# Kernel tuning notes

Hardware: AMD Instinct MI355X
Metric: run time of the kernel (lower is better)

Reference implementation:

```python
import jax, jax.numpy as jnp
import numpy as np

B, T, C, H = 32, 256, 512, 512
T_OUT = 8 * T  # fixed padded expanded length (max duration per token = 8)
ALPHA = 1.0
EPS = 1e-5


def _layer_norm(x, g, b):
    mu = jnp.mean(x, axis=-1, keepdims=True)
    var = jnp.mean(jnp.square(x - mu), axis=-1, keepdims=True)
    return (x - mu) * jax.lax.rsqrt(var + EPS) * g + b


def _conv1d_same(x, w, b):
    # x: [B,T,Cin], w: [3,Cin,Cout] -> [B,T,Cout]
    y = jax.lax.conv_general_dilated(x, w, window_strides=(1,), padding='SAME',
                                     dimension_numbers=('NWC', 'WIO', 'NWC'))
    return y + b


def setup_inputs() -> dict:
    key = jax.random.key(0)
    ks = jax.random.split(key, 8)
    s1 = 1.0 / np.sqrt(3 * C)
    s2 = 1.0 / np.sqrt(3 * H)
    return {
        'x': jax.random.normal(ks[0], (B, T, C), jnp.float32),
        'true_durations': jax.random.randint(ks[1], (B, T), 0, 8, jnp.int32),
        'W1': jax.random.normal(ks[2], (3, C, H), jnp.float32) * s1,
        'b1': jnp.zeros((H,), jnp.float32),
        'g1': jnp.ones((H,), jnp.float32),
        'beta1': jnp.zeros((H,), jnp.float32),
        'W2': jax.random.normal(ks[3], (3, H, H), jnp.float32) * s2,
        'b2': jnp.zeros((H,), jnp.float32),
        'g2': jnp.ones((H,), jnp.float32),
        'beta2': jnp.zeros((H,), jnp.float32),
        'Wl': jax.random.normal(ks[4], (H, 1), jnp.float32) * (1.0 / np.sqrt(H)),
        'bl': jnp.zeros((1,), jnp.float32),
    }


def _duration_predictor(x, W1, b1, g1, beta1, W2, b2, g2, beta2, Wl, bl):
    h = jax.nn.relu(_layer_norm(_conv1d_same(x, W1, b1), g1, beta1))
    h = jax.nn.relu(_layer_norm(_conv1d_same(h, W2, b2), g2, beta2))
    return (h @ Wl + bl)[..., 0]  # [B,T]


def _expand_by_durations(x, dur):
    # cumsum-based gather: output position t takes source token i where
    # csum[i-1] <= t < csum[i]; positions >= total length are zero-padded.
    csum = jnp.cumsum(dur, axis=-1)  # [B,T]
    pos = jnp.arange(T_OUT, dtype=csum.dtype)  # [T_OUT]
    idx = jax.vmap(lambda c: jnp.searchsorted(c, pos, side='right'))(csum)  # [B,T_OUT]
    valid = pos[None, :] < csum[:, -1:]
    idx = jnp.clip(idx, 0, dur.shape[1] - 1)
    out = jnp.take_along_axis(x, idx[..., None], axis=1)  # [B,T_OUT,C]
    return out * valid[..., None].astype(x.dtype)


def reference(x, true_durations, W1, b1, g1, beta1, W2, b2, g2, beta2, Wl, bl):
    log_lengths = _duration_predictor(x, W1, b1, g1, beta1, W2, b2, g2, beta2, Wl, bl) * ALPHA
    res = _expand_by_durations(x, true_durations)
    return res, log_lengths
```

## Files before the change

### kernel.cpp

```cpp
#include <hip/hip_runtime.h>
#include <hip/hip_bf16.h>

#define B_    32
#define T_    256
#define C_    512
#define H_    512
#define TOUT_ 2048
#define TP_   258
#define K_    1536
#define EPS_  1e-5f

typedef __attribute__((ext_vector_type(8))) short bf16x8;
typedef __attribute__((ext_vector_type(4))) float f32x4;

#define GLL16(g, l)                                                        \
  __builtin_amdgcn_global_load_lds(                                        \
      (const __attribute__((address_space(1))) void*)(g),                  \
      (__attribute__((address_space(3))) void*)(l), 16, 0, 0)

__device__ __forceinline__ void wt_convert_block(const float* __restrict__ W,
                                                 __hip_bfloat16* __restrict__ Wt,
                                                 int k0, int n0, int tid,
                                                 float* tile ) {
  const int tx = tid & 31;
  const int ty = tid >> 5;
#pragma unroll
  for (int i = 0; i < 4; ++i)
    tile[(ty * 4 + i) * 33 + tx] = W[(size_t)(k0 + ty * 4 + i) * H_ + n0 + tx];
  __syncthreads();
#pragma unroll
  for (int i = 0; i < 4; ++i)
    Wt[(size_t)(n0 + ty * 4 + i) * K_ + k0 + tx] =
        __float2bfloat16(tile[tx * 33 + ty * 4 + i]);
}

__device__ __forceinline__ void csum_block(const int* __restrict__ dur,
                                           int* __restrict__ csum,
                                           int b, int tid, int* wsum) {
  int v = dur[b * T_ + tid];
#pragma unroll
  for (int off = 1; off < 64; off <<= 1) {
    int u = __shfl_up(v, off);
    if ((tid & 63) >= off) v += u;
  }
  if ((tid & 63) == 63) wsum[tid >> 6] = v;
  __syncthreads();
  int base = 0;
#pragma unroll
  for (int j = 0; j < 4; ++j)
    if (j < (tid >> 6)) base += wsum[j];
  csum[b * T_ + tid] = v + base;
}

__device__ __forceinline__ void expand_copy_block(const float* __restrict__ X,
                                                  const int* __restrict__ csum,
                                                  float* __restrict__ res,
                                                  int u, int tid) {
  const int wave = (tid >> 6) & 3, lane = tid & 63;
#pragma unroll
  for (int k = 0; k < 4; ++k) {
    const int sr = u * 16 + wave * 4 + k;
    const int b = sr >> 8, t = sr & 255;
    const int* cb = csum + b * T_;
    const int c0 = t ? cb[t - 1] : 0;
    const int d  = cb[t] - c0;
    if (d == 0) continue;
    const float* src = X + (size_t)sr * C_;
    const float4 v0 = *(const float4*)(src + lane * 4);
    const float4 v1 = *(const float4*)(src + 256 + lane * 4);
    float* dst = res + ((size_t)b * TOUT_ + c0) * C_;
    for (int j = 0; j < d; ++j) {
      *(float4*)(dst + (size_t)j * C_ + lane * 4)       = v0;
      *(float4*)(dst + (size_t)j * C_ + 256 + lane * 4) = v1;
    }
  }
}

__device__ __forceinline__ void expand_zero_block(const int* __restrict__ csum,
                                                  float* __restrict__ res,
                                                  int z, int tid) {
  const int b  = z >> 6;
  const int t0 = (z & 63) << 5;
  const int total = csum[b * T_ + 255];
  const float4 z4 = make_float4(0.f, 0.f, 0.f, 0.f);
  const int half = (tid >> 7) & 1, c4 = tid & 127;
#pragma unroll
  for (int rr = half; rr < 32; rr += 2) {
    const int r = t0 + rr;
    if (r >= total)
      *(float4*)(res + ((size_t)b * TOUT_ + r) * C_ + c4 * 4) = z4;
  }
}

__global__ __launch_bounds__(256) void prep_kernel(const float* __restrict__ X,
                                                   const float* __restrict__ W1,
                                                   const int* __restrict__ dur,
                                                   __hip_bfloat16* __restrict__ xpad,
                                                   __hip_bfloat16* __restrict__ hpad,
                                                   __hip_bfloat16* __restrict__ Wt1,
                                                   int* __restrict__ csum) {
  __shared__ float tile[32 * 33];
  const int tid = threadIdx.x;
  if (blockIdx.x >= 4896) {
    csum_block(dur, csum, blockIdx.x - 4896, tid, (int*)tile);
    return;
  }
  if (blockIdx.x >= 4128) {
    const int id = blockIdx.x - 4128;
    wt_convert_block(W1, Wt1, (id % 48) * 32, (id / 48) * 32, tid, tile);
    return;
  }
  const int row = blockIdx.x * 2 + (tid >> 7);
  const int b = row / TP_;
  const int t = row - b * TP_;
  const int c = (tid & 127) * 4;
  __hip_bfloat16* dst = xpad + (size_t)row * C_ + c;
  if (t == 0 || t == TP_ - 1) {
    ushort4 zz = make_ushort4(0, 0, 0, 0);
    *(ushort4*)dst = zz;
    *(ushort4*)(hpad + (size_t)row * C_ + c) = zz;
    return;
  }
  const float4 v = *(const float4*)(X + (size_t)(b * T_ + t - 1) * C_ + c);
  union { __hip_bfloat16 h[4]; ushort4 u; } o;
  o.h[0] = __float2bfloat16(v.x);
  o.h[1] = __float2bfloat16(v.y);
  o.h[2] = __float2bfloat16(v.z);
  o.h[3] = __float2bfloat16(v.w);
  *(ushort4*)dst = o.u;
}

__global__ __launch_bounds__(512) void conv_expand_kernel(
    const __hip_bfloat16* __restrict__ Apad,
    const __hip_bfloat16* __restrict__ Wt,
    const float* __restrict__ bias,
    __hip_bfloat16* __restrict__ Y,
    const float* __restrict__ X,
    const int* __restrict__ csum,
    float* __restrict__ res,
    const float* __restrict__ W2,
    __hip_bfloat16* __restrict__ Wt2,
    int ex_base) {
  __shared__ __hip_bfloat16 smA[2][2][4096];
  __shared__ __hip_bfloat16 smB[2][2][4096];

  const int tid = threadIdx.x;

  if (blockIdx.x >= 896) {
    const int id = (blockIdx.x - 896) * 2 + (tid >> 8);
    float* tile = (float*)smA + (tid >> 8) * (32 * 33);
    wt_convert_block(W2, Wt2, (id % 48) * 32, (id / 48) * 32, tid & 255, tile);
    return;
  }
  if (blockIdx.x >= 256) {
    const int u = ex_base + (blockIdx.x - 256) * 2 + (tid >> 8);
    const int st = tid & 255;
    if (u < 512) expand_copy_block(X, csum, res, u, st);
    else         expand_zero_block(csum, res, u - 512, st);
    return;
  }

  const int lane = tid & 63;
  const int wid  = tid >> 6;
  const int cid  = blockIdx.x;
  const int n0 = (cid & 3) << 7;
  const int m0 = (cid >> 2) << 7;
  const int b  = m0 >> 8;
  const int t0 = m0 & 255;
  const int wm = (wid >> 2) << 6;
  const int wn = (wid & 3) << 5;

  const int rowS = tid >> 2;
  const int gsw  = ((tid & 3) + rowS) & 3;
  const __hip_bfloat16* arowA = Apad + (size_t)(b * TP_ + t0 + rowS) * C_ + (gsw << 3);
  const __hip_bfloat16* browB = Wt + (size_t)(n0 + rowS) * K_ + (gsw << 3);

  f32x4 acc[4][2] = {};

  auto stage = [&](int buf, int k0) {
    const int kw = k0 >> 9;
    const int c0 = k0 & 511;
    const __hip_bfloat16* a0 = arowA + kw * C_ + c0;
    GLL16(a0,           &smA[buf][0][tid << 3]);
    GLL16(a0 + 32,      &smA[buf][1][tid << 3]);
    GLL16(browB + k0,      &smB[buf][0][tid << 3]);
    GLL16(browB + k0 + 32, &smB[buf][1][tid << 3]);
  };

  auto compute = [&](int buf) {
    const int g   = lane >> 4;
    const int r15 = lane & 15;
    const int sa  = ((g - r15) & 3) << 3;
#pragma unroll
    for (int sl = 0; sl < 2; ++sl) {
      const __hip_bfloat16* As = smA[buf][sl];
      const __hip_bfloat16* Bs = smB[buf][sl];
      bf16x8 aF[4], bF[2];
#pragma unroll
      for (int i = 0; i < 4; ++i)
        aF[i] = *(const bf16x8*)(As + ((wm + (i << 4) + r15) << 5) + sa);
#pragma unroll
      for (int i = 0; i < 2; ++i)
        bF[i] = *(const bf16x8*)(Bs + ((wn + (i << 4) + r15) << 5) + sa);
#pragma unroll
      for (int mi = 0; mi < 4; ++mi)
#pragma unroll
        for (int ni = 0; ni < 2; ++ni)
          acc[mi][ni] = __builtin_amdgcn_mfma_f32_16x16x32_bf16(
              aF[mi], bF[ni], acc[mi][ni], 0, 0, 0);
    }
  };

  asm volatile("s_waitcnt vmcnt(0)" ::: "memory");
  stage(0, 0);
  stage(1, 64);

  for (int s = 0; s < 22; ++s) {
    asm volatile("s_waitcnt vmcnt(4)" ::: "memory");
    __builtin_amdgcn_sched_barrier(0);
    __builtin_amdgcn_s_barrier();
    compute(s & 1);
    asm volatile("s_waitcnt lgkmcnt(0)" ::: "memory");
    __builtin_amdgcn_s_barrier();
    stage(s & 1, (s + 2) << 6);
  }
  asm volatile("s_waitcnt vmcnt(4)" ::: "memory");
  __builtin_amdgcn_sched_barrier(0);
  __builtin_amdgcn_s_barrier();
  compute(0);
  asm volatile("s_waitcnt vmcnt(0)" ::: "memory");
  __builtin_amdgcn_sched_barrier(0);
  __builtin_amdgcn_s_barrier();
  compute(1);

  const int cn_base = n0 + wn + (lane & 15);
  const int rm_base = m0 + wm + ((lane >> 4) << 2);
#pragma unroll
  for (int ni = 0; ni < 2; ++ni) {
    const int cn = cn_base + (ni << 4);
    const float bb = bias[cn];
#pragma unroll
    for (int mi = 0; mi < 4; ++mi) {
#pragma unroll
      for (int rq = 0; rq < 4; ++rq) {
        const int rm = rm_base + (mi << 4) + rq;
        Y[(size_t)rm * H_ + cn] = __float2bfloat16(acc[mi][ni][rq] + bb);
      }
    }
  }
}

__global__ __launch_bounds__(256) void ln_relu_pad_kernel(
    const __hip_bfloat16* __restrict__ in,
    const float* __restrict__ g,
    const float* __restrict__ beta,
    __hip_bfloat16* __restrict__ outpad) {
  const int wave = threadIdx.x >> 6;
  const int lane = threadIdx.x & 63;
  const int row  = blockIdx.x * 4 + wave;

  const bf16x8 hv = *(const bf16x8*)(in + (size_t)row * H_ + lane * 8);
  const __hip_bfloat16* hh = (const __hip_bfloat16*)&hv;
  float f[8];
#pragma unroll
  for (int j = 0; j < 8; ++j) f[j] = __bfloat162float(hh[j]);

  float s = 0.f, q = 0.f;
#pragma unroll
  for (int j = 0; j < 8; ++j) { s += f[j]; q += f[j] * f[j]; }
#pragma unroll
  for (int off = 32; off; off >>= 1) {
    s += __shfl_xor(s, off);
    q += __shfl_xor(q, off);
  }
  const float mu  = s * (1.0f / 512.0f);
  const float var = q * (1.0f / 512.0f) - mu * mu;
  const float rs  = rsqrtf(var + EPS_);

  const float4 g0 = *(const float4*)(g + lane * 8);
  const float4 g1 = *(const float4*)(g + lane * 8 + 4);
  const float4 e0 = *(const float4*)(beta + lane * 8);
  const float4 e1 = *(const float4*)(beta + lane * 8 + 4);
  const float gg[8] = {g0.x, g0.y, g0.z, g0.w, g1.x, g1.y, g1.z, g1.w};
  const float ee[8] = {e0.x, e0.y, e0.z, e0.w, e1.x, e1.y, e1.z, e1.w};

  union { __hip_bfloat16 h[8]; bf16x8 v; } o;
#pragma unroll
  for (int j = 0; j < 8; ++j)
    o.h[j] = __float2bfloat16(fmaxf(0.f, (f[j] - mu) * rs * gg[j] + ee[j]));

  const int bq = row >> 8, t = row & 255;
  *(bf16x8*)(outpad + (size_t)(bq * TP_ + t + 1) * H_ + lane * 8) = o.v;
}

__global__ __launch_bounds__(256) void ln_relu_linear_kernel(
    const __hip_bfloat16* __restrict__ in,
    const float* __restrict__ g,
    const float* __restrict__ beta,
    const float* __restrict__ Wl,
    const float* __restrict__ bl,
    float* __restrict__ out) {
  const int wave = threadIdx.x >> 6;
  const int lane = threadIdx.x & 63;
  const int row  = blockIdx.x * 4 + wave;

  const bf16x8 hv = *(const bf16x8*)(in + (size_t)row * H_ + lane * 8);
  const __hip_bfloat16* hh = (const __hip_bfloat16*)&hv;
  float f[8];
#pragma unroll
  for (int j = 0; j < 8; ++j) f[j] = __bfloat162float(hh[j]);

  float s = 0.f, q = 0.f;
#pragma unroll
  for (int j = 0; j < 8; ++j) { s += f[j]; q += f[j] * f[j]; }
#pragma unroll
  for (int off = 32; off; off >>= 1) {
    s += __shfl_xor(s, off);
    q += __shfl_xor(q, off);
  }
  const float mu  = s * (1.0f / 512.0f);
  const float var = q * (1.0f / 512.0f) - mu * mu;
  const float rs  = rsqrtf(var + EPS_);

  const float4 g0 = *(const float4*)(g + lane * 8);
  const float4 g1 = *(const float4*)(g + lane * 8 + 4);
  const float4 e0 = *(const float4*)(beta + lane * 8);
  const float4 e1 = *(const float4*)(beta + lane * 8 + 4);
  const float4 w0 = *(const float4*)(Wl + lane * 8);
  const float4 w1 = *(const float4*)(Wl + lane * 8 + 4);
  const float gg[8] = {g0.x, g0.y, g0.z, g0.w, g1.x, g1.y, g1.z, g1.w};
  const float ee[8] = {e0.x, e0.y, e0.z, e0.w, e1.x, e1.y, e1.z, e1.w};
  const float ww[8] = {w0.x, w0.y, w0.z, w0.w, w1.x, w1.y, w1.z, w1.w};

  float sd = 0.f;
#pragma unroll
  for (int j = 0; j < 8; ++j)
    sd += fmaxf(0.f, (f[j] - mu) * rs * gg[j] + ee[j]) * ww[j];
#pragma unroll
  for (int off = 32; off; off >>= 1) sd += __shfl_xor(sd, off);

  if (lane == 0) out[row] = sd + bl[0];
}

extern "C" void kernel_launch(void* const* d_in, const int* in_sizes, int n_in,
                              void* d_out, int out_size, void* d_ws, size_t ws_size,
                              hipStream_t stream) {
  const float* x     = (const float*)d_in[0];
  const int*   dur   = (const int*)d_in[1];
  const float* W1    = (const float*)d_in[2];
  const float* b1    = (const float*)d_in[3];
  const float* g1    = (const float*)d_in[4];
  const float* beta1 = (const float*)d_in[5];
  const float* W2    = (const float*)d_in[6];
  const float* b2    = (const float*)d_in[7];
  const float* g2    = (const float*)d_in[8];
  const float* beta2 = (const float*)d_in[9];
  const float* Wl    = (const float*)d_in[10];
  const float* bl    = (const float*)d_in[11];

  float* out = (float*)d_out;
  float* res    = out;
  float* loglen = out + (size_t)B_ * TOUT_ * C_;

  char* ws = (char*)d_ws;
  __hip_bfloat16* xpad = (__hip_bfloat16*)ws;
  __hip_bfloat16* hpad = xpad + (size_t)B_ * TP_ * C_;
  __hip_bfloat16* Wt1  = hpad + (size_t)B_ * TP_ * C_;
  __hip_bfloat16* Wt2  = Wt1 + (size_t)H_ * K_;
  __hip_bfloat16* tmp  = Wt2 + (size_t)H_ * K_;
  int*   csum = (int*)(tmp + (size_t)B_ * T_ * H_);

  prep_kernel<<<4928, 256, 0, stream>>>(x, W1, dur, xpad, hpad, Wt1, csum);

  conv_expand_kernel<<<1280, 512, 0, stream>>>(xpad, Wt1, b1, tmp,
                                               x, csum, res, W2, Wt2, 0);
  ln_relu_pad_kernel<<<B_ * T_ / 4, 256, 0, stream>>>(tmp, g1, beta1, hpad);

  conv_expand_kernel<<<896, 512, 0, stream>>>(hpad, Wt2, b2, tmp,
                                              x, csum, res, nullptr, nullptr, 1280);
  ln_relu_linear_kernel<<<B_ * T_ / 4, 256, 0, stream>>>(tmp, g2, beta2, Wl, bl, loglen);
}
```

Before: 79.95 us.

## Use 256-thread blocks with 64x64 warp tiles in conv GEMM

The fused conv/expand kernel moves from 512-thread blocks with 8 waves of 64x32 tiles to 256-thread blocks with 4 waves of 64x64 tiles. Each wave now holds a 4x4 accumulator grid, which raises MFMA work per LDS fragment load. Each thread issues twice as many global-to-LDS loads, with the vmcnt waits and LDS swizzle adjusted to match. The expand and weight-convert side blocks now handle one unit per block, so the grid sizes grow. In exchange, register pressure rises and fewer waves per CU are available to hide latency.

```diff
diff --git a/kernel.cpp b/kernel.cpp
--- a/kernel.cpp
+++ b/kernel.cpp
@@ -130,7 +130,7 @@
   *(ushort4*)dst = o.u;
 }
 
-__global__ __launch_bounds__(512) void conv_expand_kernel(
+__global__ __launch_bounds__(256) void conv_expand_kernel(
     const __hip_bfloat16* __restrict__ Apad,
     const __hip_bfloat16* __restrict__ Wt,
     const float* __restrict__ bias,
@@ -146,17 +146,15 @@
 
   const int tid = threadIdx.x;
 
-  if (blockIdx.x >= 896) {
-    const int id = (blockIdx.x - 896) * 2 + (tid >> 8);
-    float* tile = (float*)smA + (tid >> 8) * (32 * 33);
-    wt_convert_block(W2, Wt2, (id % 48) * 32, (id / 48) * 32, tid & 255, tile);
+  if (blockIdx.x >= 1536) {
+    const int id = blockIdx.x - 1536;
+    wt_convert_block(W2, Wt2, (id % 48) * 32, (id / 48) * 32, tid, (float*)smA);
     return;
   }
   if (blockIdx.x >= 256) {
-    const int u = ex_base + (blockIdx.x - 256) * 2 + (tid >> 8);
-    const int st = tid & 255;
-    if (u < 512) expand_copy_block(X, csum, res, u, st);
-    else         expand_zero_block(csum, res, u - 512, st);
+    const int u = ex_base + (blockIdx.x - 256);
+    if (u < 512) expand_copy_block(X, csum, res, u, tid);
+    else         expand_zero_block(csum, res, u - 512, tid);
     return;
   }
 
@@ -167,45 +165,51 @@
   const int m0 = (cid >> 2) << 7;
   const int b  = m0 >> 8;
   const int t0 = m0 & 255;
-  const int wm = (wid >> 2) << 6;
-  const int wn = (wid & 3) << 5;
+  const int wm = (wid >> 1) << 6;
+  const int wn = (wid & 1) << 6;
 
   const int rowS = tid >> 2;
-  const int gsw  = ((tid & 3) + rowS) & 3;
-  const __hip_bfloat16* arowA = Apad + (size_t)(b * TP_ + t0 + rowS) * C_ + (gsw << 3);
-  const __hip_bfloat16* browB = Wt + (size_t)(n0 + rowS) * K_ + (gsw << 3);
-
-  f32x4 acc[4][2] = {};
+  const int gsw  = ((tid & 3) + (tid >> 3)) & 3;
+  const __hip_bfloat16* arow0 = Apad + (size_t)(b * TP_ + t0 + rowS) * C_ + (gsw << 3);
+  const __hip_bfloat16* arow1 = arow0 + (size_t)64 * C_;
+  const __hip_bfloat16* brow0 = Wt + (size_t)(n0 + rowS) * K_ + (gsw << 3);
+  const __hip_bfloat16* brow1 = brow0 + (size_t)64 * K_;
+
+  f32x4 acc[4][4] = {};
 
   auto stage = [&](int buf, int k0) {
     const int kw = k0 >> 9;
     const int c0 = k0 & 511;
-    const __hip_bfloat16* a0 = arowA + kw * C_ + c0;
-    GLL16(a0,           &smA[buf][0][tid << 3]);
-    GLL16(a0 + 32,      &smA[buf][1][tid << 3]);
-    GLL16(browB + k0,      &smB[buf][0][tid << 3]);
-    GLL16(browB + k0 + 32, &smB[buf][1][tid << 3]);
+    const __hip_bfloat16* a0 = arow0 + kw * C_ + c0;
+    const __hip_bfloat16* a1 = arow1 + kw * C_ + c0;
+    GLL16(a0,      &smA[buf][0][tid << 3]);
+    GLL16(a0 + 32, &smA[buf][1][tid << 3]);
+    GLL16(a1,      &smA[buf][0][2048 + (tid << 3)]);
+    GLL16(a1 + 32, &smA[buf][1][2048 + (tid << 3)]);
+    GLL16(brow0 + k0,      &smB[buf][0][tid << 3]);
+    GLL16(brow0 + k0 + 32, &smB[buf][1][tid << 3]);
+    GLL16(brow1 + k0,      &smB[buf][0][2048 + (tid << 3)]);
+    GLL16(brow1 + k0 + 32, &smB[buf][1][2048 + (tid << 3)]);
   };
 
   auto compute = [&](int buf) {
     const int g   = lane >> 4;
     const int r15 = lane & 15;
-    const int sa  = ((g - r15) & 3) << 3;
+    const int sa  = ((g - (r15 >> 1)) & 3) << 3;
 #pragma unroll
     for (int sl = 0; sl < 2; ++sl) {
       const __hip_bfloat16* As = smA[buf][sl];
       const __hip_bfloat16* Bs = smB[buf][sl];
-      bf16x8 aF[4], bF[2];
-#pragma unroll
-      for (int i = 0; i < 4; ++i)
+      bf16x8 aF[4], bF[4];
+#pragma unroll
+      for (int i = 0; i < 4; ++i) {
         aF[i] = *(const bf16x8*)(As + ((wm + (i << 4) + r15) << 5) + sa);
-#pragma unroll
-      for (int i = 0; i < 2; ++i)
         bF[i] = *(const bf16x8*)(Bs + ((wn + (i << 4) + r15) << 5) + sa);
+      }
 #pragma unroll
       for (int mi = 0; mi < 4; ++mi)
 #pragma unroll
-        for (int ni = 0; ni < 2; ++ni)
+        for (int ni = 0; ni < 4; ++ni)
           acc[mi][ni] = __builtin_amdgcn_mfma_f32_16x16x32_bf16(
               aF[mi], bF[ni], acc[mi][ni], 0, 0, 0);
     }
@@ -216,7 +220,7 @@
   stage(1, 64);
 
   for (int s = 0; s < 22; ++s) {
-    asm volatile("s_waitcnt vmcnt(4)" ::: "memory");
+    asm volatile("s_waitcnt vmcnt(8)" ::: "memory");
     __builtin_amdgcn_sched_barrier(0);
     __builtin_amdgcn_s_barrier();
     compute(s & 1);
@@ -224,7 +228,7 @@
     __builtin_amdgcn_s_barrier();
     stage(s & 1, (s + 2) << 6);
   }
-  asm volatile("s_waitcnt vmcnt(4)" ::: "memory");
+  asm volatile("s_waitcnt vmcnt(8)" ::: "memory");
   __builtin_amdgcn_sched_barrier(0);
   __builtin_amdgcn_s_barrier();
   compute(0);
@@ -236,7 +240,7 @@
   const int cn_base = n0 + wn + (lane & 15);
   const int rm_base = m0 + wm + ((lane >> 4) << 2);
 #pragma unroll
-  for (int ni = 0; ni < 2; ++ni) {
+  for (int ni = 0; ni < 4; ++ni) {
     const int cn = cn_base + (ni << 4);
     const float bb = bias[cn];
 #pragma unroll
@@ -372,11 +376,11 @@
 
   prep_kernel<<<4928, 256, 0, stream>>>(x, W1, dur, xpad, hpad, Wt1, csum);
 
-  conv_expand_kernel<<<1280, 512, 0, stream>>>(xpad, Wt1, b1, tmp,
+  conv_expand_kernel<<<2304, 256, 0, stream>>>(xpad, Wt1, b1, tmp,
                                                x, csum, res, W2, Wt2, 0);
   ln_relu_pad_kernel<<<B_ * T_ / 4, 256, 0, stream>>>(tmp, g1, beta1, hpad);
 
-  conv_expand_kernel<<<896, 512, 0, stream>>>(hpad, Wt2, b2, tmp,
-                                              x, csum, res, nullptr, nullptr, 1280);
+  conv_expand_kernel<<<1536, 256, 0, stream>>>(hpad, Wt2, b2, tmp,
+                                               x, csum, res, nullptr, nullptr, 1280);
   ln_relu_linear_kernel<<<B_ * T_ / 4, 256, 0, stream>>>(tmp, g2, beta2, Wl, bl, loglen);
 }
```

New measurement: 81.42 us. No clear change (+1.8%).
